# Kernel optimization log

Hardware: AMD Instinct MI355X
Metric: run time of the kernel (lower is better)

Reference implementation:

```python
import jax, jax.numpy as jnp
import numpy as np

SL, BS, HS, FFN, E, TOPK = 2048, 4, 1024, 4096, 8, 2
T = SL * BS

def setup_inputs() -> dict:
    key = jax.random.key(0)
    k1, k2, k3, k4, k5, k6 = jax.random.split(key, 6)
    x = jax.random.normal(k1, (SL, BS, HS), dtype=jnp.float32)
    expert_weights = jax.random.uniform(k2, (T, TOPK), dtype=jnp.float32)
    expert_indices = jax.random.randint(k3, (T, TOPK), 0, E).astype(jnp.int64)
    scores = jax.random.uniform(k4, (T, TOPK), dtype=jnp.float32)
    w1 = jax.random.normal(k5, (E, HS, FFN), dtype=jnp.float32) * 0.02
    w2 = jax.random.normal(k6, (E, FFN, HS), dtype=jnp.float32) * 0.02
    return {"x": x, "expert_weights": expert_weights, "scores": scores,
            "w1": w1, "w2": w2, "expert_indices": expert_indices}

def reference(x, expert_weights, scores, w1, w2, expert_indices):
    # Dropless MoE dispatch-compute-combine with router_type=None.
    # Math identity: megablocks gather/grouped-GEMM/scatter with per-copy
    # expert_weights equals, for each token t:
    #   out[t] = sum_k expert_weights[t,k] * MLP_{e(t,k)}(x[t])
    # We fold the top-k copies into a per-(token, expert) combine weight and
    # run one GEMM pair per expert (fixed small E), matching the grouped GEMM.
    sl, bs, hs = x.shape
    num_experts = w1.shape[0]
    xf = x.reshape(-1, hs)  # [T, hs]
    onehot = jax.nn.one_hot(expert_indices, num_experts, dtype=x.dtype)  # [T, k, E]
    combine = jnp.einsum("tk,tke->et", expert_weights, onehot)  # [E, T]

    def expert_step(acc, inputs):
        w1e, w2e, cw = inputs  # [hs, ffn], [ffn, hs], [T]
        h = jax.nn.gelu(xf @ w1e, approximate=False)  # [T, ffn]
        acc = acc + cw[:, None] * (h @ w2e)  # [T, hs]
        return acc, None

    out, _ = jax.lax.scan(expert_step, jnp.zeros_like(xf), (w1, w2, combine))
    return out.reshape(sl, bs, hs)
```

## Files before the change

### kernel.cpp

```cpp
#include <hip/hip_runtime.h>
#include <hip/hip_bf16.h>
#include <math.h>
#include <stdint.h>

#define N_TOK   8192
#define HS      1024
#define FFN     4096
#define NE      8
#define NA      16384
#define CAP     16384
#define BM      256
#define MAXT    72

typedef __attribute__((ext_vector_type(8))) short          bf16x8;
typedef __attribute__((ext_vector_type(4))) float          f32x4;
typedef __attribute__((ext_vector_type(4))) float          fvec4;
typedef __attribute__((ext_vector_type(4))) unsigned short usvec4;

__device__ __forceinline__ void gl_lds16(const void* g, void* l) {
  __builtin_amdgcn_global_load_lds(
      (const __attribute__((address_space(1))) unsigned int*)g,
      (__attribute__((address_space(3))) unsigned int*)l,
      16, 0, 0);
}

__device__ __forceinline__ unsigned short f2bf(float f) {
  union { float f; unsigned int u; } v; v.f = f;
  unsigned int r = v.u + 0x7FFFu + ((v.u >> 16) & 1u);
  return (unsigned short)(r >> 16);
}


__global__ void cvt_x_kernel(const fvec4* __restrict__ in, unsigned short* __restrict__ out, int n4) {
  int i = blockIdx.x * 256 + threadIdx.x;
  if (i >= n4) return;
  fvec4 v = in[i];
  usvec4 o;
  o[0] = f2bf(v[0]); o[1] = f2bf(v[1]); o[2] = f2bf(v[2]); o[3] = f2bf(v[3]);
  *(usvec4*)(out + (size_t)i * 4) = o;
}

__global__ void tpose_cvt_kernel(const float* __restrict__ in, unsigned short* __restrict__ out,
                                 int R, int C) {
  __shared__ float t[64][65];
  int bc = blockIdx.x * 64, br = blockIdx.y * 64, e = blockIdx.z;
  const float* ine = in + (size_t)e * R * C;
  unsigned short* oute = out + (size_t)e * R * C;
  int tx = threadIdx.x & 63, ty = threadIdx.x >> 6;
#pragma unroll
  for (int q = 0; q < 16; ++q) {
    int r = ty * 16 + q;
    t[r][tx] = ine[(size_t)(br + r) * C + bc + tx];
  }
  __syncthreads();
#pragma unroll
  for (int q = 0; q < 16; ++q) {
    int c = ty * 16 + q;
    oute[(size_t)(bc + c) * R + br + tx] = f2bf(t[tx][c]);
  }
}


__global__ void route_kernel(const int* __restrict__ idx, const float* __restrict__ wts,
                             int* __restrict__ counts, int* __restrict__ btok,
                             int* __restrict__ bslot, float* __restrict__ bw) {
  int a = blockIdx.x * 256 + threadIdx.x;
  if (a >= NA) return;
  int e = idx[a];
  int pos = atomicAdd(&counts[e], 1);
  btok[(size_t)e * CAP + pos]  = a >> 1;
  bslot[(size_t)e * CAP + pos] = a;
  bw[(size_t)e * CAP + pos]    = wts[a];
}

__global__ void build_tiles_kernel(int* __restrict__ counts, int2* __restrict__ table) {
  if (threadIdx.x == 0 && blockIdx.x == 0) {
    int nt = 0;
    for (int e = 0; e < NE; ++e) {
      int c = counts[e];
      int t = (c + BM - 1) >> 8;
      for (int m = 0; m < t && nt < MAXT; ++m) table[nt++] = make_int2(e, m);
    }
    counts[8] = nt;
  }
}

template <int NWN, int EPI, int KDIM, int NOUT>
__global__ __launch_bounds__(NWN * 128, 2)
void moe_gemm(const unsigned short* __restrict__ Ab,
              const unsigned short* __restrict__ Bb,
              unsigned short* __restrict__ hout,
              float* __restrict__ perm,
              const int* __restrict__ btok,
              const int* __restrict__ bslot,
              const float* __restrict__ bw,
              const int* __restrict__ counts,
              const int2* __restrict__ table,
              int p0, int tc) {
  constexpr int NWAVES = 2 * NWN;
  constexpr int BN_ = NWN * 64;
  constexpr int NBLK = NOUT / BN_;
  constexpr int NCH = 16 + BN_ / 16;
  constexpr int CPW = NCH / NWAVES;
  constexpr int BUFSZ = 16384 + BN_ * 64;
  constexpr int NT = KDIM / 32;

  __shared__ char lds[3 * BUFSZ];

  int bid = blockIdx.x;
  int xcd = bid & 7, slot = bid >> 3;
  int j = xcd + 8 * (slot / NBLK);
  int bn0 = (slot % NBLK) * BN_;

  int nt = counts[8];
  if (j < p0 || j >= p0 + tc || j >= nt) return;
  int2 te = table[j];
  int e = te.x, tm = te.y;
  int count = counts[e];
  int slotb = j - p0;

  int tid = threadIdx.x;
  int wid = tid >> 6, lane = tid & 63;
  int wm = wid / NWN, wn = wid % NWN;

  const unsigned short* Be = Bb + (size_t)e * ((size_t)FFN * HS);

  const char* src[CPW];
  int dst[CPW];
#pragma unroll
  for (int q = 0; q < CPW; ++q) {
    int c = wid * CPW + q;
    int rr = (c < 16 ? c * 16 : (c - 16) * 16) + (lane >> 2);
    int klog = ((lane & 3) * 16) ^ (((rr >> 1) & 3) << 4);
    if (c < 16) {
      dst[q] = c * 1024;
      if (EPI == 0) {
        int grow = tm * BM + rr;
        int tok = (grow < count) ? btok[(size_t)e * CAP + grow] : 0;
        src[q] = (const char*)(Ab + (size_t)tok * KDIM) + klog;
      } else {
        src[q] = (const char*)(Ab + ((size_t)slotb * BM + rr) * KDIM) + klog;
      }
    } else {
      dst[q] = 16384 + (c - 16) * 1024;
      src[q] = (const char*)(Be + (size_t)(bn0 + rr) * KDIM) + klog;
    }
  }

  int rA = wm * 128 + (lane & 15);
  int rB = wn * 64 + (lane & 15);
  int ks = (lane >> 4) * 16;
  int offA0 = rA * 64 + (ks ^ (((rA >> 1) & 3) << 4));
  int offB0 = 16384 + rB * 64 + (ks ^ (((rB >> 1) & 3) << 4));

  f32x4 acc[8][4] = {};

#pragma unroll
  for (int q = 0; q < CPW; ++q) gl_lds16(src[q], lds + dst[q]);
#pragma unroll
  for (int q = 0; q < CPW; ++q) gl_lds16(src[q] + 64, lds + BUFSZ + dst[q]);

  int bi = 0;
  for (int t = 0; t < NT; ++t) {
    if constexpr (CPW == 4) asm volatile("s_waitcnt vmcnt(4)" ::: "memory");
    else                    asm volatile("s_waitcnt vmcnt(6)" ::: "memory");
    __builtin_amdgcn_sched_barrier(0);
    __builtin_amdgcn_s_barrier();
    __builtin_amdgcn_sched_barrier(0);

    int kt2 = t + 2; if (kt2 >= NT) kt2 -= NT;
    int bi2 = bi + 2; if (bi2 >= 3) bi2 -= 3;
    char* db = lds + bi2 * BUFSZ;
#pragma unroll
    for (int q = 0; q < CPW; ++q)
      gl_lds16(src[q] + (size_t)kt2 * 64, db + dst[q]);

    const char* rbuf = lds + bi * BUFSZ;
    bf16x8 a[8], b[4];
    b[0] = *(const bf16x8*)(rbuf + offB0);
    b[1] = *(const bf16x8*)(rbuf + offB0 + 1024);
    b[2] = *(const bf16x8*)(rbuf + offB0 + 2048);
    b[3] = *(const bf16x8*)(rbuf + offB0 + 3072);
    a[0] = *(const bf16x8*)(rbuf + offA0);
    a[1] = *(const bf16x8*)(rbuf + offA0 + 1024);
    __builtin_amdgcn_sched_barrier(0);
    a[2] = *(const bf16x8*)(rbuf + offA0 + 2048);
    a[3] = *(const bf16x8*)(rbuf + offA0 + 3072);
    __builtin_amdgcn_sched_barrier(0);
    a[4] = *(const bf16x8*)(rbuf + offA0 + 4096);
    a[5] = *(const bf16x8*)(rbuf + offA0 + 5120);
    __builtin_amdgcn_sched_barrier(0);
    a[6] = *(const bf16x8*)(rbuf + offA0 + 6144);
    a[7] = *(const bf16x8*)(rbuf + offA0 + 7168);
    __builtin_amdgcn_sched_barrier(0);
    __builtin_amdgcn_s_setprio(1);
#pragma unroll
    for (int g = 0; g < 4; ++g) {
#pragma unroll
      for (int i = 2 * g; i < 2 * g + 2; ++i)
#pragma unroll
        for (int n = 0; n < 4; ++n)
          acc[i][n] = __builtin_amdgcn_mfma_f32_16x16x32_bf16(a[i], b[n], acc[i][n], 0, 0, 0);
      __builtin_amdgcn_sched_barrier(0);
    }
    __builtin_amdgcn_s_setprio(0);
    ++bi; if (bi >= 3) bi = 0;
  }

  if (EPI == 0) {
    size_t hb = (size_t)slotb * BM;
#pragma unroll
    for (int i = 0; i < 8; ++i) {
      int row = wm * 128 + i * 16 + ((lane >> 4) << 2);
#pragma unroll
      for (int n = 0; n < 4; ++n) {
        int col = bn0 + wn * 64 + n * 16 + (lane & 15);
#pragma unroll
        for (int r = 0; r < 4; ++r) {
          float v = acc[i][n][r];
          float x2 = v * v;
          float u2 = 1.5957691216057308f * v * fmaf(0.044715f, x2, 1.0f);
          u2 = fminf(fmaxf(u2, -30.f), 30.f);
          float ee = __expf(u2);
          float g = v * __fdividef(ee, ee + 1.0f);
          hout[(hb + row + r) * FFN + col] = f2bf(g);
        }
      }
    }
  } else {
#pragma unroll
    for (int i = 0; i < 8; ++i) {
      int rowb = wm * 128 + i * 16 + ((lane >> 4) << 2);
#pragma unroll
      for (int r = 0; r < 4; ++r) {
        int grow = tm * BM + rowb + r;
        if (grow < count) {
          int s = bslot[(size_t)e * CAP + grow];
          float wgt = bw[(size_t)e * CAP + grow];
#pragma unroll
          for (int n = 0; n < 4; ++n) {
            int col = bn0 + wn * 64 + n * 16 + (lane & 15);
            perm[(size_t)s * HS + col] = wgt * acc[i][n][r];
          }
        }
      }
    }
  }
}

__global__ void combine_kernel(const fvec4* __restrict__ perm, fvec4* __restrict__ out, int n4) {
  int i = blockIdx.x * 256 + threadIdx.x;
  if (i >= n4) return;
  int t = i >> 8;
  int c = i & 255;
  out[i] = perm[(size_t)(2 * t) * 256 + c] + perm[(size_t)(2 * t + 1) * 256 + c];
}


extern "C" void kernel_launch(void* const* d_in, const int* in_sizes, int n_in,
                              void* d_out, int out_size, void* d_ws, size_t ws_size,
                              hipStream_t stream) {
  const float* x   = (const float*)d_in[0];
  const float* ew  = (const float*)d_in[1];
  const float* w1  = (const float*)d_in[3];
  const float* w2  = (const float*)d_in[4];
  const int*   eix = (const int*)d_in[5];

  char* ws = (char*)d_ws;
  const size_t o_w1T    = 0;
  const size_t o_w2T    = 67108864ULL;
  const size_t o_xb     = 134217728ULL;
  const size_t o_btok   = 150994944ULL;
  const size_t o_bslot  = 151519232ULL;
  const size_t o_bw     = 152043520ULL;
  const size_t o_counts = 152567808ULL;
  const size_t o_table  = 152568064ULL;
  const size_t o_perm   = 152569344ULL;
  const size_t o_h      = 219678208ULL;

  unsigned short* w1T = (unsigned short*)(ws + o_w1T);
  unsigned short* w2T = (unsigned short*)(ws + o_w2T);
  unsigned short* xb  = (unsigned short*)(ws + o_xb);
  int*   btok   = (int*)(ws + o_btok);
  int*   bslot  = (int*)(ws + o_bslot);
  float* bw     = (float*)(ws + o_bw);
  int*   counts = (int*)(ws + o_counts);
  int2*  table  = (int2*)(ws + o_table);
  float* perm   = (float*)(ws + o_perm);
  unsigned short* hbuf = (unsigned short*)(ws + o_h);

  long long havail = (long long)ws_size - (long long)o_h;
  long long tile_bytes = (long long)BM * FFN * 2;
  int tc = (int)(havail / tile_bytes);
  if (tc < 1) tc = 1;
  if (tc > MAXT) tc = MAXT;
  int npass = (MAXT + tc - 1) / tc;

  hipMemsetAsync(counts, 0, 256, stream);

  cvt_x_kernel<<<(N_TOK * HS / 4 + 255) / 256, 256, 0, stream>>>(
      (const fvec4*)x, xb, N_TOK * HS / 4);
  tpose_cvt_kernel<<<dim3(FFN / 64, HS / 64, NE), 256, 0, stream>>>(w1, w1T, HS, FFN);
  tpose_cvt_kernel<<<dim3(HS / 64, FFN / 64, NE), 256, 0, stream>>>(w2, w2T, FFN, HS);

  route_kernel<<<(NA + 255) / 256, 256, 0, stream>>>(eix, ew, counts, btok, bslot, bw);
  build_tiles_kernel<<<1, 64, 0, stream>>>(counts, table);

  for (int p = 0; p < npass; ++p) {
    moe_gemm<4, 0, HS, FFN><<<dim3(MAXT * 16), 512, 0, stream>>>(
        xb, w1T, hbuf, perm, btok, bslot, bw, counts, table, p * tc, tc);
    moe_gemm<2, 1, FFN, HS><<<dim3(MAXT * 8), 256, 0, stream>>>(
        hbuf, w2T, hbuf, perm, btok, bslot, bw, counts, table, p * tc, tc);
  }

  combine_kernel<<<(N_TOK * HS / 4 + 255) / 256, 256, 0, stream>>>(
      (const fvec4*)perm, (fvec4*)d_out, N_TOK * HS / 4);
}
```

Baseline: 608.4 us.

## Split GEMM K-step into four barrier-synchronized phases interleaving loads with MFMAs

Restructures the main GEMM loop into four phases. Each phase issues a slice of the global-to-LDS prefetch and a pair of A-fragment LDS reads, then runs 8 MFMAs between workgroup barriers, so memory traffic is spread across the iteration instead of bunched at its start. The vmcnt wait moves to the end of each iteration, with one wait before the loop and one drain after it. This adds eight barriers per K-step, which may cost more in synchronization than the improved interleaving recovers.

```diff
diff --git a/kernel.cpp b/kernel.cpp
--- a/kernel.cpp
+++ b/kernel.cpp
@@ -159,53 +159,101 @@
   for (int q = 0; q < CPW; ++q) gl_lds16(src[q], lds + dst[q]);
 #pragma unroll
   for (int q = 0; q < CPW; ++q) gl_lds16(src[q] + 64, lds + BUFSZ + dst[q]);
+  if constexpr (CPW == 4) asm volatile("s_waitcnt vmcnt(4)" ::: "memory");
+  else                    asm volatile("s_waitcnt vmcnt(6)" ::: "memory");
+  __builtin_amdgcn_sched_barrier(0);
+  __builtin_amdgcn_s_barrier();
+  __builtin_amdgcn_sched_barrier(0);
+
+#define MFMA_ROW(I, AV, B0, B1, B2, B3)                                          \
+  acc[I][0] = __builtin_amdgcn_mfma_f32_16x16x32_bf16(AV, B0, acc[I][0], 0, 0, 0); \
+  acc[I][1] = __builtin_amdgcn_mfma_f32_16x16x32_bf16(AV, B1, acc[I][1], 0, 0, 0); \
+  acc[I][2] = __builtin_amdgcn_mfma_f32_16x16x32_bf16(AV, B2, acc[I][2], 0, 0, 0); \
+  acc[I][3] = __builtin_amdgcn_mfma_f32_16x16x32_bf16(AV, B3, acc[I][3], 0, 0, 0);
+
+#define PHASE_SYNC_PRE                                                           \
+  __builtin_amdgcn_sched_barrier(0);                                             \
+  __builtin_amdgcn_s_barrier();                                                  \
+  __builtin_amdgcn_sched_barrier(0);                                             \
+  asm volatile("s_waitcnt lgkmcnt(0)" ::: "memory");                             \
+  __builtin_amdgcn_sched_barrier(0);
+
+#define PHASE_SYNC_POST                                                          \
+  __builtin_amdgcn_sched_barrier(0);                                             \
+  __builtin_amdgcn_s_barrier();                                                  \
+  __builtin_amdgcn_sched_barrier(0);
 
   int bi = 0;
   for (int t = 0; t < NT; ++t) {
-    if constexpr (CPW == 4) asm volatile("s_waitcnt vmcnt(4)" ::: "memory");
-    else                    asm volatile("s_waitcnt vmcnt(6)" ::: "memory");
-    __builtin_amdgcn_sched_barrier(0);
-    __builtin_amdgcn_s_barrier();
-    __builtin_amdgcn_sched_barrier(0);
-
     int kt2 = t + 2; if (kt2 >= NT) kt2 -= NT;
     int bi2 = bi + 2; if (bi2 >= 3) bi2 -= 3;
     char* db = lds + bi2 * BUFSZ;
-#pragma unroll
-    for (int q = 0; q < CPW; ++q)
-      gl_lds16(src[q] + (size_t)kt2 * 64, db + dst[q]);
-
     const char* rbuf = lds + bi * BUFSZ;
-    bf16x8 a[8], b[4];
-    b[0] = *(const bf16x8*)(rbuf + offB0);
-    b[1] = *(const bf16x8*)(rbuf + offB0 + 1024);
-    b[2] = *(const bf16x8*)(rbuf + offB0 + 2048);
-    b[3] = *(const bf16x8*)(rbuf + offB0 + 3072);
-    a[0] = *(const bf16x8*)(rbuf + offA0);
-    a[1] = *(const bf16x8*)(rbuf + offA0 + 1024);
-    __builtin_amdgcn_sched_barrier(0);
-    a[2] = *(const bf16x8*)(rbuf + offA0 + 2048);
-    a[3] = *(const bf16x8*)(rbuf + offA0 + 3072);
-    __builtin_amdgcn_sched_barrier(0);
-    a[4] = *(const bf16x8*)(rbuf + offA0 + 4096);
-    a[5] = *(const bf16x8*)(rbuf + offA0 + 5120);
-    __builtin_amdgcn_sched_barrier(0);
-    a[6] = *(const bf16x8*)(rbuf + offA0 + 6144);
-    a[7] = *(const bf16x8*)(rbuf + offA0 + 7168);
-    __builtin_amdgcn_sched_barrier(0);
+    bf16x8 b0, b1, b2, b3, pa0, pa1;
+
+    b0  = *(const bf16x8*)(rbuf + offB0);
+    b1  = *(const bf16x8*)(rbuf + offB0 + 1024);
+    b2  = *(const bf16x8*)(rbuf + offB0 + 2048);
+    b3  = *(const bf16x8*)(rbuf + offB0 + 3072);
+    pa0 = *(const bf16x8*)(rbuf + offA0);
+    pa1 = *(const bf16x8*)(rbuf + offA0 + 1024);
+    gl_lds16(src[0] + (size_t)kt2 * 64, db + dst[0]);
+    if constexpr (CPW == 6) gl_lds16(src[1] + (size_t)kt2 * 64, db + dst[1]);
+    PHASE_SYNC_PRE
     __builtin_amdgcn_s_setprio(1);
-#pragma unroll
-    for (int g = 0; g < 4; ++g) {
-#pragma unroll
-      for (int i = 2 * g; i < 2 * g + 2; ++i)
-#pragma unroll
-        for (int n = 0; n < 4; ++n)
-          acc[i][n] = __builtin_amdgcn_mfma_f32_16x16x32_bf16(a[i], b[n], acc[i][n], 0, 0, 0);
-      __builtin_amdgcn_sched_barrier(0);
-    }
+    MFMA_ROW(0, pa0, b0, b1, b2, b3)
+    MFMA_ROW(1, pa1, b0, b1, b2, b3)
     __builtin_amdgcn_s_setprio(0);
+    PHASE_SYNC_POST
+
+    pa0 = *(const bf16x8*)(rbuf + offA0 + 2048);
+    pa1 = *(const bf16x8*)(rbuf + offA0 + 3072);
+    if constexpr (CPW == 6) {
+      gl_lds16(src[2] + (size_t)kt2 * 64, db + dst[2]);
+      gl_lds16(src[3] + (size_t)kt2 * 64, db + dst[3]);
+    } else {
+      gl_lds16(src[1] + (size_t)kt2 * 64, db + dst[1]);
+    }
+    PHASE_SYNC_PRE
+    __builtin_amdgcn_s_setprio(1);
+    MFMA_ROW(2, pa0, b0, b1, b2, b3)
+    MFMA_ROW(3, pa1, b0, b1, b2, b3)
+    __builtin_amdgcn_s_setprio(0);
+    PHASE_SYNC_POST
+
+    pa0 = *(const bf16x8*)(rbuf + offA0 + 4096);
+    pa1 = *(const bf16x8*)(rbuf + offA0 + 5120);
+    if constexpr (CPW == 6) {
+      gl_lds16(src[4] + (size_t)kt2 * 64, db + dst[4]);
+    } else {
+      gl_lds16(src[2] + (size_t)kt2 * 64, db + dst[2]);
+    }
+    PHASE_SYNC_PRE
+    __builtin_amdgcn_s_setprio(1);
+    MFMA_ROW(4, pa0, b0, b1, b2, b3)
+    MFMA_ROW(5, pa1, b0, b1, b2, b3)
+    __builtin_amdgcn_s_setprio(0);
+    PHASE_SYNC_POST
+
+    pa0 = *(const bf16x8*)(rbuf + offA0 + 6144);
+    pa1 = *(const bf16x8*)(rbuf + offA0 + 7168);
+    if constexpr (CPW == 6) {
+      gl_lds16(src[5] + (size_t)kt2 * 64, db + dst[5]);
+    } else {
+      gl_lds16(src[3] + (size_t)kt2 * 64, db + dst[3]);
+    }
+    PHASE_SYNC_PRE
+    __builtin_amdgcn_s_setprio(1);
+    MFMA_ROW(6, pa0, b0, b1, b2, b3)
+    MFMA_ROW(7, pa1, b0, b1, b2, b3)
+    __builtin_amdgcn_s_setprio(0);
+    if constexpr (CPW == 4) asm volatile("s_waitcnt vmcnt(4)" ::: "memory");
+    else                    asm volatile("s_waitcnt vmcnt(6)" ::: "memory");
+    PHASE_SYNC_POST
+
     ++bi; if (bi >= 3) bi = 0;
   }
+  asm volatile("s_waitcnt vmcnt(0)" ::: "memory");
 
   if (EPI == 0) {
     size_t hb = (size_t)slotb * BM;
@@ -246,6 +294,9 @@
       }
     }
   }
+#undef MFMA_ROW
+#undef PHASE_SYNC_PRE
+#undef PHASE_SYNC_POST
 }
 
 __global__ void combine_kernel(const fvec4* __restrict__ perm, fvec4* __restrict__ out, int n4) {
```

Result: no change. 615.5 us (+1.2%).

## Use 256x256 tiles with 4 waves and split-K for second GEMM

Applied to the files above, without the earlier changes.

Both grouped GEMMs now use a uniform 256x256 output tile computed by 4 waves, each holding 128x128 accumulators (8x8 MFMA fragments), so every LDS fragment is reused more often. The second GEMM splits K=4096 in two halves, keeping the block count while tiles grow, and writes partial results to two separate permutation buffers that the combine kernel adds. A-fragment loads are interleaved with the MFMA loop instead of issued up front. The cost is higher register pressure (occupancy 1), an extra 64MB partial buffer with more combine traffic, and a smaller workspace left for h, which may force more passes.

```diff
diff --git a/kernel.cpp b/kernel.cpp
--- a/kernel.cpp
+++ b/kernel.cpp
@@ -11,6 +11,7 @@
 #define CAP     16384
 #define BM      256
 #define MAXT    72
+#define PERMSZ  16777216ULL
 
 typedef __attribute__((ext_vector_type(8))) short          bf16x8;
 typedef __attribute__((ext_vector_type(4))) float          f32x4;
@@ -85,8 +86,8 @@
   }
 }
 
-template <int NWN, int EPI, int KDIM, int NOUT>
-__global__ __launch_bounds__(NWN * 128, 2)
+template <int EPI, int KROW, int NT>
+__global__ __launch_bounds__(256, 1)
 void moe_gemm(const unsigned short* __restrict__ Ab,
               const unsigned short* __restrict__ Bb,
               unsigned short* __restrict__ hout,
@@ -97,20 +98,17 @@
               const int* __restrict__ counts,
               const int2* __restrict__ table,
               int p0, int tc) {
-  constexpr int NWAVES = 2 * NWN;
-  constexpr int BN_ = NWN * 64;
-  constexpr int NBLK = NOUT / BN_;
-  constexpr int NCH = 16 + BN_ / 16;
-  constexpr int CPW = NCH / NWAVES;
-  constexpr int BUFSZ = 16384 + BN_ * 64;
-  constexpr int NT = KDIM / 32;
-
+  constexpr int BUFSZ = 32768;
+  constexpr int SPT = (EPI == 0) ? 16 : 8;
   __shared__ char lds[3 * BUFSZ];
 
   int bid = blockIdx.x;
   int xcd = bid & 7, slot = bid >> 3;
-  int j = xcd + 8 * (slot / NBLK);
-  int bn0 = (slot % NBLK) * BN_;
+  int j = xcd + 8 * (slot / SPT);
+  int r0 = slot % SPT;
+  int kq  = (EPI == 0) ? 0 : (r0 >> 2);
+  int bn0 = (EPI == 0) ? r0 * 256 : (r0 & 3) * 256;
+  int kbyte0 = kq * (NT * 64);
 
   int nt = counts[8];
   if (j < p0 || j >= p0 + tc || j >= nt) return;
@@ -121,15 +119,15 @@
 
   int tid = threadIdx.x;
   int wid = tid >> 6, lane = tid & 63;
-  int wm = wid / NWN, wn = wid % NWN;
+  int wm = wid >> 1, wn = wid & 1;
 
   const unsigned short* Be = Bb + (size_t)e * ((size_t)FFN * HS);
 
-  const char* src[CPW];
-  int dst[CPW];
-#pragma unroll
-  for (int q = 0; q < CPW; ++q) {
-    int c = wid * CPW + q;
+  const char* src[8];
+  int dst[8];
+#pragma unroll
+  for (int q = 0; q < 8; ++q) {
+    int c = wid * 8 + q;
     int rr = (c < 16 ? c * 16 : (c - 16) * 16) + (lane >> 2);
     int klog = ((lane & 3) * 16) ^ (((rr >> 1) & 3) << 4);
     if (c < 16) {
@@ -137,33 +135,32 @@
       if (EPI == 0) {
         int grow = tm * BM + rr;
         int tok = (grow < count) ? btok[(size_t)e * CAP + grow] : 0;
-        src[q] = (const char*)(Ab + (size_t)tok * KDIM) + klog;
+        src[q] = (const char*)(Ab + (size_t)tok * KROW) + kbyte0 + klog;
       } else {
-        src[q] = (const char*)(Ab + ((size_t)slotb * BM + rr) * KDIM) + klog;
+        src[q] = (const char*)(Ab + ((size_t)slotb * BM + rr) * KROW) + kbyte0 + klog;
       }
     } else {
       dst[q] = 16384 + (c - 16) * 1024;
-      src[q] = (const char*)(Be + (size_t)(bn0 + rr) * KDIM) + klog;
+      src[q] = (const char*)(Be + (size_t)(bn0 + rr) * KROW) + kbyte0 + klog;
     }
   }
 
   int rA = wm * 128 + (lane & 15);
-  int rB = wn * 64 + (lane & 15);
+  int rB = wn * 128 + (lane & 15);
   int ks = (lane >> 4) * 16;
   int offA0 = rA * 64 + (ks ^ (((rA >> 1) & 3) << 4));
   int offB0 = 16384 + rB * 64 + (ks ^ (((rB >> 1) & 3) << 4));
 
-  f32x4 acc[8][4] = {};
-
-#pragma unroll
-  for (int q = 0; q < CPW; ++q) gl_lds16(src[q], lds + dst[q]);
-#pragma unroll
-  for (int q = 0; q < CPW; ++q) gl_lds16(src[q] + 64, lds + BUFSZ + dst[q]);
+  f32x4 acc[8][8] = {};
+
+#pragma unroll
+  for (int q = 0; q < 8; ++q) gl_lds16(src[q], lds + dst[q]);
+#pragma unroll
+  for (int q = 0; q < 8; ++q) gl_lds16(src[q] + 64, lds + BUFSZ + dst[q]);
 
   int bi = 0;
   for (int t = 0; t < NT; ++t) {
-    if constexpr (CPW == 4) asm volatile("s_waitcnt vmcnt(4)" ::: "memory");
-    else                    asm volatile("s_waitcnt vmcnt(6)" ::: "memory");
+    asm volatile("s_waitcnt vmcnt(8)" ::: "memory");
     __builtin_amdgcn_sched_barrier(0);
     __builtin_amdgcn_s_barrier();
     __builtin_amdgcn_sched_barrier(0);
@@ -172,40 +169,27 @@
     int bi2 = bi + 2; if (bi2 >= 3) bi2 -= 3;
     char* db = lds + bi2 * BUFSZ;
 #pragma unroll
-    for (int q = 0; q < CPW; ++q)
+    for (int q = 0; q < 8; ++q)
       gl_lds16(src[q] + (size_t)kt2 * 64, db + dst[q]);
 
     const char* rbuf = lds + bi * BUFSZ;
-    bf16x8 a[8], b[4];
-    b[0] = *(const bf16x8*)(rbuf + offB0);
-    b[1] = *(const bf16x8*)(rbuf + offB0 + 1024);
-    b[2] = *(const bf16x8*)(rbuf + offB0 + 2048);
-    b[3] = *(const bf16x8*)(rbuf + offB0 + 3072);
+    bf16x8 a[8], b[8];
+#pragma unroll
+    for (int n = 0; n < 8; ++n) b[n] = *(const bf16x8*)(rbuf + offB0 + n * 1024);
     a[0] = *(const bf16x8*)(rbuf + offA0);
     a[1] = *(const bf16x8*)(rbuf + offA0 + 1024);
-    __builtin_amdgcn_sched_barrier(0);
-    a[2] = *(const bf16x8*)(rbuf + offA0 + 2048);
-    a[3] = *(const bf16x8*)(rbuf + offA0 + 3072);
-    __builtin_amdgcn_sched_barrier(0);
-    a[4] = *(const bf16x8*)(rbuf + offA0 + 4096);
-    a[5] = *(const bf16x8*)(rbuf + offA0 + 5120);
-    __builtin_amdgcn_sched_barrier(0);
-    a[6] = *(const bf16x8*)(rbuf + offA0 + 6144);
-    a[7] = *(const bf16x8*)(rbuf + offA0 + 7168);
-    __builtin_amdgcn_sched_barrier(0);
     __builtin_amdgcn_s_setprio(1);
 #pragma unroll
-    for (int g = 0; g < 4; ++g) {
-#pragma unroll
-      for (int i = 2 * g; i < 2 * g + 2; ++i)
-#pragma unroll
-        for (int n = 0; n < 4; ++n)
-          acc[i][n] = __builtin_amdgcn_mfma_f32_16x16x32_bf16(a[i], b[n], acc[i][n], 0, 0, 0);
-      __builtin_amdgcn_sched_barrier(0);
+    for (int i = 0; i < 8; ++i) {
+      if (i < 6) a[i + 2] = *(const bf16x8*)(rbuf + offA0 + (i + 2) * 1024);
+#pragma unroll
+      for (int n = 0; n < 8; ++n)
+        acc[i][n] = __builtin_amdgcn_mfma_f32_16x16x32_bf16(a[i], b[n], acc[i][n], 0, 0, 0);
     }
     __builtin_amdgcn_s_setprio(0);
     ++bi; if (bi >= 3) bi = 0;
   }
+  asm volatile("s_waitcnt vmcnt(0)" ::: "memory");
 
   if (EPI == 0) {
     size_t hb = (size_t)slotb * BM;
@@ -213,34 +197,35 @@
     for (int i = 0; i < 8; ++i) {
       int row = wm * 128 + i * 16 + ((lane >> 4) << 2);
 #pragma unroll
-      for (int n = 0; n < 4; ++n) {
-        int col = bn0 + wn * 64 + n * 16 + (lane & 15);
-#pragma unroll
-        for (int r = 0; r < 4; ++r) {
-          float v = acc[i][n][r];
+      for (int n = 0; n < 8; ++n) {
+        int col = bn0 + wn * 128 + n * 16 + (lane & 15);
+#pragma unroll
+        for (int rr = 0; rr < 4; ++rr) {
+          float v = acc[i][n][rr];
           float x2 = v * v;
           float u2 = 1.5957691216057308f * v * fmaf(0.044715f, x2, 1.0f);
           u2 = fminf(fmaxf(u2, -30.f), 30.f);
           float ee = __expf(u2);
           float g = v * __fdividef(ee, ee + 1.0f);
-          hout[(hb + row + r) * FFN + col] = f2bf(g);
+          hout[(hb + row + rr) * FFN + col] = f2bf(g);
         }
       }
     }
   } else {
+    float* pq = perm + (size_t)kq * PERMSZ;
 #pragma unroll
     for (int i = 0; i < 8; ++i) {
       int rowb = wm * 128 + i * 16 + ((lane >> 4) << 2);
 #pragma unroll
-      for (int r = 0; r < 4; ++r) {
-        int grow = tm * BM + rowb + r;
+      for (int rr = 0; rr < 4; ++rr) {
+        int grow = tm * BM + rowb + rr;
         if (grow < count) {
           int s = bslot[(size_t)e * CAP + grow];
           float wgt = bw[(size_t)e * CAP + grow];
 #pragma unroll
-          for (int n = 0; n < 4; ++n) {
-            int col = bn0 + wn * 64 + n * 16 + (lane & 15);
-            perm[(size_t)s * HS + col] = wgt * acc[i][n][r];
+          for (int n = 0; n < 8; ++n) {
+            int col = bn0 + wn * 128 + n * 16 + (lane & 15);
+            pq[(size_t)s * HS + col] = wgt * acc[i][n][rr];
           }
         }
       }
@@ -253,7 +238,11 @@
   if (i >= n4) return;
   int t = i >> 8;
   int c = i & 255;
-  out[i] = perm[(size_t)(2 * t) * 256 + c] + perm[(size_t)(2 * t + 1) * 256 + c];
+  const fvec4* p0 = perm;
+  const fvec4* p1 = perm + PERMSZ / 4;
+  size_t r0 = (size_t)(2 * t) * 256 + c;
+  size_t r1 = (size_t)(2 * t + 1) * 256 + c;
+  out[i] = (p0[r0] + p1[r0]) + (p0[r1] + p1[r1]);
 }
 
 
@@ -276,7 +265,7 @@
   const size_t o_counts = 152567808ULL;
   const size_t o_table  = 152568064ULL;
   const size_t o_perm   = 152569344ULL;
-  const size_t o_h      = 219678208ULL;
+  const size_t o_h      = 286787072ULL;
 
   unsigned short* w1T = (unsigned short*)(ws + o_w1T);
   unsigned short* w2T = (unsigned short*)(ws + o_w2T);
@@ -307,9 +296,9 @@
   build_tiles_kernel<<<1, 64, 0, stream>>>(counts, table);
 
   for (int p = 0; p < npass; ++p) {
-    moe_gemm<4, 0, HS, FFN><<<dim3(MAXT * 16), 512, 0, stream>>>(
+    moe_gemm<0, HS, HS / 32><<<dim3(MAXT * 16), 256, 0, stream>>>(
         xb, w1T, hbuf, perm, btok, bslot, bw, counts, table, p * tc, tc);
-    moe_gemm<2, 1, FFN, HS><<<dim3(MAXT * 8), 256, 0, stream>>>(
+    moe_gemm<1, FFN, FFN / 64><<<dim3(MAXT * 8), 256, 0, stream>>>(
         hbuf, w2T, hbuf, perm, btok, bslot, bw, counts, table, p * tc, tc);
   }
 
```

Result: slower. 1.353 ms (+122.4%).
